# Kernel tuning notes

Measured on AMD Instinct MI355X. Metric: run time of the kernel, lower is better.

The kernel has to match this reference:

```python
import jax, jax.numpy as jnp
import numpy as np

B, N = 4, 65536
NUM_GROUP, GROUP_SIZE = 512, 64
EMB = 60


def setup_inputs() -> dict:
    key = jax.random.key(0)
    ks = jax.random.split(key, 8)
    inp = {
        'xyz': jax.random.uniform(ks[0], (B, N, 3), jnp.float32),
        'color': jax.random.uniform(ks[1], (B, N, 3), jnp.float32),
        'W1': jax.random.normal(ks[2], (6, 64), jnp.float32) * 0.2,
        'b1': jnp.zeros((64,), jnp.float32),
        'W2': jax.random.normal(ks[3], (64, 128), jnp.float32) * 0.1,
        'b2': jnp.zeros((128,), jnp.float32),
        'W3': jax.random.normal(ks[4], (128, 256), jnp.float32) * 0.08,
        'b3': jnp.zeros((256,), jnp.float32),
        'W4': jax.random.normal(ks[5], (256, 512), jnp.float32) * 0.06,
        'b4': jnp.zeros((512,), jnp.float32),
        'Wp': jax.random.normal(ks[6], (512, EMB), jnp.float32) * 0.04,
        'bp': jnp.zeros((EMB,), jnp.float32),
    }
    return inp


def fps(xyz, n):
    """Farthest point sampling. xyz: (B,N,3) -> centers (B,n,3)."""
    b, npts, _ = xyz.shape
    start = jnp.zeros((b,), jnp.int32)
    d0 = jnp.full((b, npts), 1e10, xyz.dtype)

    def step(carry, _):
        dists, last = carry
        p = jnp.take_along_axis(xyz, last[:, None, None], axis=1)  # (B,1,3)
        d = jnp.sum((xyz - p) ** 2, axis=-1)                       # (B,N)
        dists = jnp.minimum(dists, d)
        nxt = jnp.argmax(dists, axis=-1).astype(jnp.int32)
        return (dists, nxt), nxt

    (_, _), rest = jax.lax.scan(step, (d0, start), None, length=n - 1)
    idx = jnp.concatenate([start[:, None], rest.T], axis=1)        # (B,n)
    return jax.vmap(lambda pts, i: pts[i])(xyz, idx)


def knn_idx(k, xyz, new_xyz):
    """Indices of k nearest points in xyz for each query in new_xyz.
    xyz: (B,N,3), new_xyz: (B,S,3) -> (B,S,k) int32. Matches
    square_distance + topk(largest=False)."""
    sq = (jnp.sum(new_xyz ** 2, -1)[..., None]
          + jnp.sum(xyz ** 2, -1)[:, None, :]
          - 2.0 * jnp.einsum('bsc,bnc->bsn', new_xyz, xyz))        # (B,S,N)
    _, idx = jax.lax.top_k(-sq, k)
    return idx


def reference(xyz, color, W1, b1, W2, b2, W3, b3, W4, b4, Wp, bp):
    # --- Group: FPS centers + KNN neighborhood gather + centering ---
    center = fps(xyz, NUM_GROUP)                                   # (B,G,3)
    idx = knn_idx(GROUP_SIZE, xyz, center)                         # (B,G,M)
    gather = jax.vmap(lambda pts, i: pts[i])                       # pts[(B,)N,3], i (G,M)
    neighborhood = gather(xyz, idx) - center[:, :, None, :]        # (B,G,M,3) centered
    neighborhood_color = gather(color, idx)                        # (B,G,M,3)
    feats = jnp.concatenate([neighborhood, neighborhood_color], -1)  # (B,G,M,6)

    # --- PointNet: per-point MLP -> max over group -> projection ---
    x = jax.nn.relu(feats @ W1 + b1)
    x = jax.nn.relu(x @ W2 + b2)
    x = jax.nn.relu(x @ W3 + b3)
    x = jax.nn.relu(x @ W4 + b4)                                   # (B,G,M,512)
    x = jnp.max(x, axis=2)                                         # (B,G,512)
    emb = x @ Wp + bp                                              # (B,G,60)
    return emb, center
```

## Files before the change

### kernel.cpp

```cpp
#include <hip/hip_runtime.h>
#include <stdint.h>

#define DI __device__ __forceinline__

typedef _Float16 f16x8 __attribute__((ext_vector_type(8)));
typedef float f32x4 __attribute__((ext_vector_type(4)));
typedef unsigned long long u64;

constexpr int kB = 4;
constexpr int kN = 65536;
constexpr int kG = 512;
constexpr int kM = 64;
constexpr int kE = 60;
constexpr int GRD = 20;
constexpr int NCELL = GRD * GRD * GRD;
constexpr float CW = 1.0f / 20.0f;

constexpr int FPS_SUB = 8;
constexpr int FPS_TPB = 256;
constexpr int FPS_PT_T = kN / FPS_SUB / FPS_TPB;
constexpr int NFPS = kB * FPS_SUB;
constexpr int NWORK = 448;
constexpr int NBLK = NFPS + NWORK;

constexpr size_t OFF_FKEY   = 0;
constexpr size_t OFF_CCNT   = OFF_FKEY + (size_t)kB * kG * FPS_SUB * 4 * 8;
constexpr size_t OFF_GS     = OFF_CCNT + (size_t)kB * NCELL * 4;
constexpr size_t ZERO_BYTES = OFF_GS + 64;
constexpr size_t OFF_CSTART = (ZERO_BYTES + 255) & ~(size_t)255;
constexpr size_t OFF_CUR    = OFF_CSTART + (size_t)kB * (NCELL + 1) * 4;
constexpr size_t OFF_SW1    = ((OFF_CUR + (size_t)kB * NCELL * 4) + 255) & ~(size_t)255;
constexpr size_t OFF_SW2    = OFF_SW1 + 2048 * 2;
constexpr size_t OFF_SW3    = OFF_SW2 + 8192 * 2;
constexpr size_t OFF_SW4    = OFF_SW3 + 32768 * 2;
constexpr size_t OFF_WPT    = OFF_SW4 + 131072 * 2;
constexpr size_t OFF_SORT   = ((OFF_WPT + 60 * 512 * 4) + 255) & ~(size_t)255;

DI int cellof(float x) {
  int c = (int)(x * (float)GRD);
  return min(GRD - 1, max(0, c));
}
DI unsigned orderable(float f) {
  unsigned u = __float_as_uint(f);
  return (u & 0x80000000u) ? ~u : (u | 0x80000000u);
}

__global__ void k_zero(uint32_t* p, int nwords) {
  int i = blockIdx.x * blockDim.x + threadIdx.x;
  int st = gridDim.x * blockDim.x;
  for (; i < nwords; i += st) p[i] = 0u;
}

DI void swz(const float* __restrict__ W, _Float16* __restrict__ sw,
            int total, int nks, int Kreal, int N, int i0, int st) {
  for (int i = i0; i < total; i += st) {
    int j = i & 7, lane = (i >> 3) & 63, rest = i >> 9;
    int ks = rest % nks, nt = rest / nks;
    int k = ks * 32 + ((lane >> 4) << 3) + j;
    int n = nt * 16 + (lane & 15);
    sw[i] = (_Float16)((k < Kreal) ? W[k * N + n] : 0.f);
  }
}

__global__ void k_prep(const float* __restrict__ W1, const float* __restrict__ W2,
                       const float* __restrict__ W3, const float* __restrict__ W4,
                       const float* __restrict__ Wp,
                       _Float16* __restrict__ sw1, _Float16* __restrict__ sw2,
                       _Float16* __restrict__ sw3, _Float16* __restrict__ sw4,
                       float* __restrict__ wpt) {
  int i0 = blockIdx.x * blockDim.x + threadIdx.x;
  int st = gridDim.x * blockDim.x;
  swz(W1, sw1, 2048, 1, 6, 64, i0, st);
  swz(W2, sw2, 8192, 2, 64, 128, i0, st);
  swz(W3, sw3, 32768, 4, 128, 256, i0, st);
  swz(W4, sw4, 131072, 8, 256, 512, i0, st);
  for (int i = i0; i < 60 * 512; i += st) { int n = i >> 9, k = i & 511; wpt[i] = Wp[k * 60 + n]; }
}

DI void gbar(uint32_t* ctr, unsigned target) {
  __syncthreads();
  if (threadIdx.x == 0) {
    __hip_atomic_fetch_add(ctr, 1u, __ATOMIC_ACQ_REL, __HIP_MEMORY_SCOPE_AGENT);
    long bail = 0;
    while (__hip_atomic_load(ctr, __ATOMIC_ACQUIRE, __HIP_MEMORY_SCOPE_AGENT) < target) {
      __builtin_amdgcn_s_sleep(32);
      if (++bail > 100000000L) break;
    }
  }
  __syncthreads();
}

DI void fps_block(const float* __restrict__ xyz, float* __restrict__ outC,
                  u64* __restrict__ fkey, int bi) {
  const int b = bi / FPS_SUB, sub = bi % FPS_SUB;
  const int tid = threadIdx.x;
  const int wave = tid >> 6, lane = tid & 63;
  const float* X = xyz + (size_t)b * kN * 3;
  float px[FPS_PT_T], py[FPS_PT_T], pz[FPS_PT_T], dd[FPS_PT_T];
#pragma unroll
  for (int j = 0; j < FPS_PT_T; ++j) {
    int p = sub * (kN / FPS_SUB) + j * FPS_TPB + tid;
    px[j] = X[3 * p]; py[j] = X[3 * p + 1]; pz[j] = X[3 * p + 2];
    dd[j] = 1e10f;
  }
  float lx = X[0], ly = X[1], lz = X[2];
  if (sub == 0 && tid == 0) {
    outC[(size_t)b * kG * 3 + 0] = lx;
    outC[(size_t)b * kG * 3 + 1] = ly;
    outC[(size_t)b * kG * 3 + 2] = lz;
  }
  __shared__ u64 s_key[4];
  __shared__ float s_x[4], s_y[4], s_z[4];
  __shared__ float4 sp;
  u64* keyB = fkey + (size_t)b * kG * (FPS_SUB * 4);

  for (int it = 1; it < kG; ++it) {
    float bnd = -1.0f, bx = 0.f, by = 0.f, bz = 0.f;
    int bp = 0;
#pragma unroll
    for (int j = 0; j < FPS_PT_T; ++j) {
      float dx = __fsub_rn(px[j], lx);
      float dy = __fsub_rn(py[j], ly);
      float dz = __fsub_rn(pz[j], lz);
      float d = __fadd_rn(__fadd_rn(__fmul_rn(dx, dx), __fmul_rn(dy, dy)), __fmul_rn(dz, dz));
      float nd = fminf(dd[j], d);
      dd[j] = nd;
      int p = sub * (kN / FPS_SUB) + j * FPS_TPB + tid;
      if (nd > bnd) { bnd = nd; bx = px[j]; by = py[j]; bz = pz[j]; bp = p; }
    }
    u64 best = ((u64)__float_as_uint(bnd) << 32) | (unsigned)(0xFFFFFFFFu - (unsigned)bp);
#pragma unroll
    for (int off = 32; off; off >>= 1) {
      u64 ok = __shfl_down(best, (unsigned)off);
      float ox = __shfl_down(bx, (unsigned)off);
      float oy = __shfl_down(by, (unsigned)off);
      float oz = __shfl_down(bz, (unsigned)off);
      if (ok > best) { best = ok; bx = ox; by = oy; bz = oz; }
    }
    if (lane == 0) { s_key[wave] = best; s_x[wave] = bx; s_y[wave] = by; s_z[wave] = bz; }
    __syncthreads();
    if (wave == 0) {
      int i4 = lane & 3;
      u64 kk = s_key[i4]; float kx = s_x[i4], ky = s_y[i4], kz = s_z[i4];
#pragma unroll
      for (int off = 2; off; off >>= 1) {
        u64 ok = __shfl_down(kk, (unsigned)off);
        float ox = __shfl_down(kx, (unsigned)off);
        float oy = __shfl_down(ky, (unsigned)off);
        float oz = __shfl_down(kz, (unsigned)off);
        if (ok > kk) { kk = ok; kx = ox; ky = oy; kz = oz; }
      }
      u64* slots = keyB + (size_t)it * (FPS_SUB * 4);
      if (lane == 0) {
        u64 tag = (unsigned)it;
        u64* my = slots + sub * 4;
        __hip_atomic_store(my + 1, ((u64)__float_as_uint(kx) << 32) | tag,
                           __ATOMIC_RELAXED, __HIP_MEMORY_SCOPE_AGENT);
        __hip_atomic_store(my + 2, ((u64)__float_as_uint(ky) << 32) | tag,
                           __ATOMIC_RELAXED, __HIP_MEMORY_SCOPE_AGENT);
        __hip_atomic_store(my + 3, ((u64)__float_as_uint(kz) << 32) | tag,
                           __ATOMIC_RELAXED, __HIP_MEMORY_SCOPE_AGENT);
        __hip_atomic_store(my + 0, kk, __ATOMIC_RELAXED, __HIP_MEMORY_SCOPE_AGENT);
      }
      u64 v = 0; bool okp; long bail = 0;
      do {
        if (lane < FPS_SUB * 4)
          v = __hip_atomic_load(slots + lane, __ATOMIC_RELAXED, __HIP_MEMORY_SCOPE_AGENT);
        okp = (lane >= FPS_SUB * 4) ||
              ((lane & 3) ? ((unsigned)v == (unsigned)it) : (v != 0ull));
      } while (!__all(okp) && ++bail < 200000000L);
      u64 key = (lane < FPS_SUB * 4 && (lane & 3) == 0) ? v : 0ull;
      int slot = lane >> 2;
#pragma unroll
      for (int off = 16; off >= 4; off >>= 1) {
        u64 ok = __shfl_down(key, (unsigned)off);
        int os = __shfl_down(slot, (unsigned)off);
        if (ok > key) { key = ok; slot = os; }
      }
      slot = __shfl(slot, 0);
      u64 vx = __shfl(v, slot * 4 + 1);
      u64 vy = __shfl(v, slot * 4 + 2);
      u64 vz = __shfl(v, slot * 4 + 3);
      if (lane == 0) {
        float wxc = __uint_as_float((unsigned)(vx >> 32));
        float wyc = __uint_as_float((unsigned)(vy >> 32));
        float wzc = __uint_as_float((unsigned)(vz >> 32));
        sp = make_float4(wxc, wyc, wzc, 0.f);
        if (sub == 0) {
          outC[((size_t)b * kG + it) * 3 + 0] = wxc;
          outC[((size_t)b * kG + it) * 3 + 1] = wyc;
          outC[((size_t)b * kG + it) * 3 + 2] = wzc;
        }
      }
    }
    __syncthreads();
    lx = sp.x; ly = sp.y; lz = sp.z;
  }
}

DI void bitonic(u64* a, int n, int tid) {
  for (int k = 2; k <= n; k <<= 1)
    for (int j = k >> 1; j > 0; j >>= 1) {
      __syncthreads();
      for (int i = tid; i < n; i += 256) {
        int ix = i ^ j;
        if (ix > i) {
          u64 x = a[i], y = a[ix];
          bool up = ((i & k) == 0);
          if ((x > y) == up) { a[i] = y; a[ix] = x; }
        }
      }
    }
  __syncthreads();
}

template <int Kdim, int Ndim, int SIN, int SOUT>
DI void mfma_layer(const _Float16* __restrict__ Xin, _Float16* __restrict__ Xout,
                   const _Float16* __restrict__ Wsw, const float* __restrict__ bias,
                   int wave, int lane) {
  constexpr int NKS = Kdim / 32;
  constexpr int NTW = Ndim / 64;
  constexpr int CH = (NTW < 4) ? NTW : 4;
  const int quad = lane >> 4, l16 = lane & 15;
  for (int c0 = 0; c0 < NTW; c0 += CH) {
    f32x4 acc[CH][4];
#pragma unroll
    for (int nt = 0; nt < CH; ++nt) {
      float bv = bias[wave * (Ndim / 4) + (c0 + nt) * 16 + l16];
#pragma unroll
      for (int m = 0; m < 4; ++m) acc[nt][m] = {bv, bv, bv, bv};
    }
#pragma unroll
    for (int ks = 0; ks < NKS; ++ks) {
      f16x8 af[4];
#pragma unroll
      for (int m = 0; m < 4; ++m)
        af[m] = *(const f16x8*)(Xin + (m * 16 + l16) * SIN + ks * 32 + quad * 8);
#pragma unroll
      for (int nt = 0; nt < CH; ++nt) {
        int ntg = wave * NTW + c0 + nt;
        f16x8 bf = *(const f16x8*)(Wsw + ((size_t)(ntg * NKS + ks) * 64 + lane) * 8);
#pragma unroll
        for (int m = 0; m < 4; ++m)
          acc[nt][m] = __builtin_amdgcn_mfma_f32_16x16x32_f16(af[m], bf, acc[nt][m], 0, 0, 0);
      }
    }
#pragma unroll
    for (int nt = 0; nt < CH; ++nt) {
      int col = wave * (Ndim / 4) + (c0 + nt) * 16 + l16;
#pragma unroll
      for (int m = 0; m < 4; ++m)
#pragma unroll
        for (int r = 0; r < 4; ++r) {
          int row = m * 16 + quad * 4 + r;
          Xout[row * SOUT + col] = (_Float16)fmaxf(acc[nt][m][r], 0.f);
        }
    }
  }
}

DI void mfma_layer4(const _Float16* __restrict__ Xin, const _Float16* __restrict__ Wsw,
                    const float* __restrict__ bias, float* __restrict__ maxv,
                    int wave, int lane) {
  constexpr int SIN = 264, NKS = 8, NTW = 8, CH = 4;
  const int quad = lane >> 4, l16 = lane & 15;
  for (int c0 = 0; c0 < NTW; c0 += CH) {
    f32x4 acc[CH][4];
#pragma unroll
    for (int nt = 0; nt < CH; ++nt) {
      float bv = bias[wave * 128 + (c0 + nt) * 16 + l16];
#pragma unroll
      for (int m = 0; m < 4; ++m) acc[nt][m] = {bv, bv, bv, bv};
    }
#pragma unroll
    for (int ks = 0; ks < NKS; ++ks) {
      f16x8 af[4];
#pragma unroll
      for (int m = 0; m < 4; ++m)
        af[m] = *(const f16x8*)(Xin + (m * 16 + l16) * SIN + ks * 32 + quad * 8);
#pragma unroll
      for (int nt = 0; nt < CH; ++nt) {
        int ntg = wave * NTW + c0 + nt;
        f16x8 bf = *(const f16x8*)(Wsw + ((size_t)(ntg * NKS + ks) * 64 + lane) * 8);
#pragma unroll
        for (int m = 0; m < 4; ++m)
          acc[nt][m] = __builtin_amdgcn_mfma_f32_16x16x32_f16(af[m], bf, acc[nt][m], 0, 0, 0);
      }
    }
#pragma unroll
    for (int nt = 0; nt < CH; ++nt) {
      float mx = 0.f;
#pragma unroll
      for (int m = 0; m < 4; ++m)
#pragma unroll
        for (int r = 0; r < 4; ++r) mx = fmaxf(mx, acc[nt][m][r]);
      mx = fmaxf(mx, __shfl_xor(mx, 16, 64));
      mx = fmaxf(mx, __shfl_xor(mx, 32, 64));
      if (quad == 0) maxv[wave * 128 + (c0 + nt) * 16 + l16] = mx;
    }
  }
}

__global__ __launch_bounds__(256, 2) void k_fused(
    const float* __restrict__ xyz, const float* __restrict__ color,
    float* __restrict__ outC, float* __restrict__ outE,
    u64* __restrict__ fkey, uint32_t* __restrict__ ccnt,
    uint32_t* __restrict__ cstart, uint32_t* __restrict__ cur,
    float4* __restrict__ sorted, uint32_t* __restrict__ gs,
    const _Float16* __restrict__ sw1, const _Float16* __restrict__ sw2,
    const _Float16* __restrict__ sw3, const _Float16* __restrict__ sw4,
    const float* __restrict__ wpt,
    const float* __restrict__ b1, const float* __restrict__ b2,
    const float* __restrict__ b3, const float* __restrict__ b4,
    const float* __restrict__ bp) {
  const int bi = blockIdx.x;
  if (bi < NFPS) { fps_block(xyz, outC, fkey, bi); return; }

  const int wj = bi - NFPS;
  const int tid = threadIdx.x;
  const int wave = tid >> 6, lane = tid & 63;
  __shared__ __align__(16) char smem[65536];
  __shared__ int nC;
  __shared__ float4 spc;
  __shared__ uint32_t s_part[256];
  u64* cand = (u64*)smem;

  for (int i = wj * 256 + tid; i < kB * kN; i += NWORK * 256) {
    int b = i >> 16, p = i & (kN - 1);
    const float* q = xyz + ((size_t)b * kN + p) * 3;
    int cid = (cellof(q[2]) * GRD + cellof(q[1])) * GRD + cellof(q[0]);
    atomicAdd(&ccnt[b * NCELL + cid], 1u);
  }
  gbar(gs + 0, NWORK);
  if (wj < kB) {
    int b = wj;
    const uint32_t* cc = ccnt + (size_t)b * NCELL;
    uint32_t* cs = cstart + (size_t)b * (NCELL + 1);
    uint32_t* cu = cur + (size_t)b * NCELL;
    const int chunk = 32;
    int c0 = tid * chunk;
    uint32_t s = 0;
    for (int i = 0; i < chunk; ++i) { int c = c0 + i; if (c < NCELL) s += cc[c]; }
    s_part[tid] = s;
    __syncthreads();
    for (int off = 1; off < 256; off <<= 1) {
      uint32_t add = (tid >= off) ? s_part[tid - off] : 0u;
      __syncthreads();
      s_part[tid] += add;
      __syncthreads();
    }
    uint32_t run = s_part[tid] - s;
    for (int i = 0; i < chunk; ++i) {
      int c = c0 + i;
      if (c < NCELL) { cs[c] = run; cu[c] = run; run += cc[c]; }
    }
    if (tid == 255) cs[NCELL] = run;
  }
  gbar(gs + 1, NWORK);
  for (int i = wj * 256 + tid; i < kB * kN; i += NWORK * 256) {
    int b = i >> 16, p = i & (kN - 1);
    const float* q = xyz + ((size_t)b * kN + p) * 3;
    float x = q[0], y = q[1], z = q[2];
    int cid = (cellof(z) * GRD + cellof(y)) * GRD + cellof(x);
    uint32_t pos = atomicAdd(&cur[b * NCELL + cid], 1u);
    sorted[(size_t)b * kN + pos] = make_float4(x, y, z, __uint_as_float((unsigned)p));
  }
  gbar(gs + 2, NWORK);

  for (int j = wj; j < kB * kG; j += NWORK) {
    const int it = j >> 2, b = j & 3;
    const float* X = xyz + (size_t)b * kN * 3;
    if (it == 0) {
      if (tid == 0) spc = make_float4(X[0], X[1], X[2], 0.f);
    } else if (tid < 64) {
      const u64* slots = fkey + ((size_t)b * kG + it) * (FPS_SUB * 4);
      const int pl = tid;
      u64 v = 0; bool okp; long bail = 0;
      for (;;) {
        if (pl < FPS_SUB * 4)
          v = __hip_atomic_load(slots + pl, __ATOMIC_RELAXED, __HIP_MEMORY_SCOPE_AGENT);
        okp = (pl >= FPS_SUB * 4) ||
              ((pl & 3) ? ((unsigned)v == (unsigned)it) : (v != 0ull));
        if (__all(okp)) break;
        __builtin_amdgcn_s_sleep(127);
        if (++bail > 50000000L) break;
      }
      u64 key = (pl < FPS_SUB * 4 && (pl & 3) == 0) ? v : 0ull;
      int slot = pl >> 2;
#pragma unroll
      for (int off = 16; off >= 4; off >>= 1) {
        u64 ok = __shfl_down(key, (unsigned)off);
        int os = __shfl_down(slot, (unsigned)off);
        if (ok > key) { key = ok; slot = os; }
      }
      slot = __shfl(slot, 0);
      u64 vx = __shfl(v, slot * 4 + 1);
      u64 vy = __shfl(v, slot * 4 + 2);
      u64 vz = __shfl(v, slot * 4 + 3);
      if (pl == 0)
        spc = make_float4(__uint_as_float((unsigned)(vx >> 32)),
                          __uint_as_float((unsigned)(vy >> 32)),
                          __uint_as_float((unsigned)(vz >> 32)), 0.f);
    }
    __syncthreads();
    const float cx = spc.x, cy = spc.y, cz = spc.z;

    const float nc = __fadd_rn(__fadd_rn(__fmul_rn(cx, cx), __fmul_rn(cy, cy)), __fmul_rn(cz, cz));
    const float4* SP = sorted + (size_t)b * kN;
    const uint32_t* CS = cstart + (size_t)b * (NCELL + 1);
    const int ccx = cellof(cx), ccy = cellof(cy), ccz = cellof(cz);
    if (tid == 0) nC = 0;
    __syncthreads();
    int plox = 1, phix = 0, ploy = 1, phiy = 0, ploz = 1, phiz = 0;
    for (int r = 1; r <= GRD; ++r) {
      int lox = max(0, ccx - r), hix = min(GRD - 1, ccx + r);
      int loy = max(0, ccy - r), hiy = min(GRD - 1, ccy + r);
      int loz = max(0, ccz - r), hiz = min(GRD - 1, ccz + r);
      for (int z = loz; z <= hiz; ++z)
        for (int y = loy; y <= hiy; ++y) {
          bool rowPrev = (r > 1) && (z >= ploz && z <= phiz && y >= ploy && y <= phiy);
          for (int s = 0; s < 2; ++s) {
            int xa, xb;
            if (!rowPrev) { if (s) break; xa = lox; xb = hix; }
            else if (s == 0) { xa = lox; xb = plox - 1; }
            else { xa = phix + 1; xb = hix; }
            if (xa > xb) continue;
            int c0 = (z * GRD + y) * GRD + xa;
            int i0 = CS[c0];
            int i1 = CS[(z * GRD + y) * GRD + xb + 1];
            for (int i = i0 + tid; i < i1; i += 256) {
              float4 pt = SP[i];
              float npn = __fadd_rn(__fadd_rn(__fmul_rn(pt.x, pt.x), __fmul_rn(pt.y, pt.y)),
                                    __fmul_rn(pt.z, pt.z));
              float dot = __fadd_rn(__fadd_rn(__fmul_rn(cx, pt.x), __fmul_rn(cy, pt.y)),
                                    __fmul_rn(cz, pt.z));
              float sq = __fsub_rn(__fadd_rn(nc, npn), __fmul_rn(2.0f, dot));
              unsigned key = orderable(sq);
              int pos = atomicAdd(&nC, 1);
              if (pos < 8192)
                cand[pos] = ((u64)key << 32) | (unsigned)__float_as_uint(pt.w);
            }
          }
        }
      __syncthreads();
      int n = min(nC, 8192);
      float rc = 1e30f;
      if (lox > 0) rc = fminf(rc, cx - (float)lox * CW);
      if (hix < GRD - 1) rc = fminf(rc, (float)(hix + 1) * CW - cx);
      if (loy > 0) rc = fminf(rc, cy - (float)loy * CW);
      if (hiy < GRD - 1) rc = fminf(rc, (float)(hiy + 1) * CW - cy);
      if (loz > 0) rc = fminf(rc, cz - (float)loz * CW);
      if (hiz < GRD - 1) rc = fminf(rc, (float)(hiz + 1) * CW - cz);
      float r2 = (rc >= 1e29f) ? 3.0e38f : rc * rc * (1.0f - 1e-5f);
      unsigned keyR = orderable(r2);
      bool done = false;
      if (n >= kM) {
        int np2 = 1;
        while (np2 < n) np2 <<= 1;
        for (int i = n + tid; i < np2; i += 256) cand[i] = ~0ull;
        bitonic(cand, np2, tid);
        unsigned k63 = (unsigned)(cand[kM - 1] >> 32);
        done = (k63 <= keyR);
        if (tid == 0) nC = n;
      }
      __syncthreads();
      if (done) break;
      plox = lox; phix = hix; ploy = loy; phiy = hiy; ploz = loz; phiz = hiz;
    }

    uint32_t pidx = 0;
    if (tid < kM) pidx = (uint32_t)(cand[tid] & 0xFFFFFFFFu);
    __syncthreads();
    _Float16* bufA = (_Float16*)smem;
    _Float16* bufB = (_Float16*)(smem + 17408);
    float* maxv = (float*)smem;
    float* psum = (float*)(smem + 2048);
    if (tid < kM) {
      const float* xp = xyz + ((size_t)b * kN + pidx) * 3;
      const float* cp = color + ((size_t)b * kN + pidx) * 3;
      f16x8 v = {};
      v[0] = (_Float16)__fsub_rn(xp[0], cx);
      v[1] = (_Float16)__fsub_rn(xp[1], cy);
      v[2] = (_Float16)__fsub_rn(xp[2], cz);
      v[3] = (_Float16)cp[0];
      v[4] = (_Float16)cp[1];
      v[5] = (_Float16)cp[2];
      f16x8 zf = {};
      *(f16x8*)(bufA + tid * 40 + 0) = v;
      *(f16x8*)(bufA + tid * 40 + 8) = zf;
      *(f16x8*)(bufA + tid * 40 + 16) = zf;
      *(f16x8*)(bufA + tid * 40 + 24) = zf;
    }
    __syncthreads();
    mfma_layer<32, 64, 40, 72>(bufA, bufB, sw1, b1, wave, lane);
    __syncthreads();
    mfma_layer<64, 128, 72, 136>(bufB, bufA, sw2, b2, wave, lane);
    __syncthreads();
    mfma_layer<128, 256, 136, 264>(bufA, bufB, sw3, b3, wave, lane);
    __syncthreads();
    mfma_layer4(bufB, sw4, b4, maxv, wave, lane);
    __syncthreads();
    if (tid < 240) {
      int jj = tid >> 2, q = tid & 3;
      const float* w = wpt + (size_t)jj * 512 + q * 128;
      float s = 0.f;
#pragma unroll 4
      for (int k = 0; k < 128; ++k) s = fmaf(maxv[q * 128 + k], w[k], s);
      psum[tid] = s;
    }
    __syncthreads();
    if (tid < kE) {
      float e = __fadd_rn(__fadd_rn(psum[tid * 4 + 0], psum[tid * 4 + 1]),
                          __fadd_rn(psum[tid * 4 + 2], psum[tid * 4 + 3])) + bp[tid];
      outE[((size_t)b * kG + it) * kE + tid] = e;
    }
    __syncthreads();
  }
}

extern "C" void kernel_launch(void* const* d_in, const int* in_sizes, int n_in,
                              void* d_out, int out_size, void* d_ws, size_t ws_size,
                              hipStream_t stream) {
  (void)in_sizes; (void)n_in; (void)out_size; (void)ws_size;
  const float* xyz = (const float*)d_in[0];
  const float* color = (const float*)d_in[1];
  const float* W1 = (const float*)d_in[2];
  const float* b1 = (const float*)d_in[3];
  const float* W2 = (const float*)d_in[4];
  const float* b2 = (const float*)d_in[5];
  const float* W3 = (const float*)d_in[6];
  const float* b3 = (const float*)d_in[7];
  const float* W4 = (const float*)d_in[8];
  const float* b4 = (const float*)d_in[9];
  const float* Wp = (const float*)d_in[10];
  const float* bp = (const float*)d_in[11];

  char* ws = (char*)d_ws;
  auto fkey = (u64*)(ws + OFF_FKEY);
  auto ccnt = (uint32_t*)(ws + OFF_CCNT);
  auto gs = (uint32_t*)(ws + OFF_GS);
  auto cstart = (uint32_t*)(ws + OFF_CSTART);
  auto cur = (uint32_t*)(ws + OFF_CUR);
  auto sw1 = (_Float16*)(ws + OFF_SW1);
  auto sw2 = (_Float16*)(ws + OFF_SW2);
  auto sw3 = (_Float16*)(ws + OFF_SW3);
  auto sw4 = (_Float16*)(ws + OFF_SW4);
  auto wpt = (float*)(ws + OFF_WPT);
  auto sorted = (float4*)(ws + OFF_SORT);

  float* outE = (float*)d_out;
  float* outC = outE + (size_t)kB * kG * kE;

  k_zero<<<128, 256, 0, stream>>>((uint32_t*)ws, (int)(ZERO_BYTES / 4));
  k_prep<<<256, 256, 0, stream>>>(W1, W2, W3, W4, Wp, sw1, sw2, sw3, sw4, wpt);
  k_fused<<<NBLK, 256, 0, stream>>>(xyz, color, outC, outE, fkey, ccnt, cstart, cur,
                                    sorted, gs, sw1, sw2, sw3, sw4, wpt,
                                    b1, b2, b3, b4, bp);
}
```

Baseline: 2.128 ms.

## Replace brute-force multi-block FPS with single-block chunk-pruned FPS over grid-sorted points

```diff
diff --git a/kernel.cpp b/kernel.cpp
--- a/kernel.cpp
+++ b/kernel.cpp
@@ -6,6 +6,7 @@
 typedef _Float16 f16x8 __attribute__((ext_vector_type(8)));
 typedef float f32x4 __attribute__((ext_vector_type(4)));
 typedef unsigned long long u64;
+typedef unsigned short u16;
 
 constexpr int kB = 4;
 constexpr int kN = 65536;
@@ -16,20 +17,18 @@
 constexpr int NCELL = GRD * GRD * GRD;
 constexpr float CW = 1.0f / 20.0f;
 
-constexpr int FPS_SUB = 8;
-constexpr int FPS_TPB = 256;
-constexpr int FPS_PT_T = kN / FPS_SUB / FPS_TPB;
-constexpr int NFPS = kB * FPS_SUB;
-constexpr int NWORK = 448;
+constexpr int NCH = 2048;
+constexpr int CHSZ = 32;
+constexpr int NFPS = kB;
+constexpr int NWORK = 508;
 constexpr int NBLK = NFPS + NWORK;
 
-constexpr size_t OFF_FKEY   = 0;
-constexpr size_t OFF_CCNT   = OFF_FKEY + (size_t)kB * kG * FPS_SUB * 4 * 8;
-constexpr size_t OFF_GS     = OFF_CCNT + (size_t)kB * NCELL * 4;
-constexpr size_t ZERO_BYTES = OFF_GS + 64;
+constexpr size_t OFF_CLINE  = 0;
+constexpr size_t OFF_GRDY   = (size_t)kB * kG * 128;
+constexpr size_t ZERO_BYTES = OFF_GRDY + 64;
 constexpr size_t OFF_CSTART = (ZERO_BYTES + 255) & ~(size_t)255;
-constexpr size_t OFF_CUR    = OFF_CSTART + (size_t)kB * (NCELL + 1) * 4;
-constexpr size_t OFF_SW1    = ((OFF_CUR + (size_t)kB * NCELL * 4) + 255) & ~(size_t)255;
+constexpr size_t OFF_DD     = (OFF_CSTART + (size_t)kB * (NCELL + 1) * 4 + 255) & ~(size_t)255;
+constexpr size_t OFF_SW1    = (OFF_DD + (size_t)kB * kN * 4 + 255) & ~(size_t)255;
 constexpr size_t OFF_SW2    = OFF_SW1 + 2048 * 2;
 constexpr size_t OFF_SW3    = OFF_SW2 + 8192 * 2;
 constexpr size_t OFF_SW4    = OFF_SW3 + 32768 * 2;
@@ -43,6 +42,16 @@
 DI unsigned orderable(float f) {
   unsigned u = __float_as_uint(f);
   return (u & 0x80000000u) ? ~u : (u | 0x80000000u);
+}
+DI _Float16 f16dn(float v) {
+  _Float16 h = (_Float16)v;
+  if ((float)h > v) h = __builtin_bit_cast(_Float16, (u16)(__builtin_bit_cast(u16, h) - 1));
+  return h;
+}
+DI _Float16 f16up(float v) {
+  _Float16 h = (_Float16)v;
+  if ((float)h < v) h = __builtin_bit_cast(_Float16, (u16)(__builtin_bit_cast(u16, h) + 1));
+  return h;
 }
 
 __global__ void k_zero(uint32_t* p, int nwords) {
@@ -77,127 +86,6 @@
   for (int i = i0; i < 60 * 512; i += st) { int n = i >> 9, k = i & 511; wpt[i] = Wp[k * 60 + n]; }
 }
 
-DI void gbar(uint32_t* ctr, unsigned target) {
-  __syncthreads();
-  if (threadIdx.x == 0) {
-    __hip_atomic_fetch_add(ctr, 1u, __ATOMIC_ACQ_REL, __HIP_MEMORY_SCOPE_AGENT);
-    long bail = 0;
-    while (__hip_atomic_load(ctr, __ATOMIC_ACQUIRE, __HIP_MEMORY_SCOPE_AGENT) < target) {
-      __builtin_amdgcn_s_sleep(32);
-      if (++bail > 100000000L) break;
-    }
-  }
-  __syncthreads();
-}
-
-DI void fps_block(const float* __restrict__ xyz, float* __restrict__ outC,
-                  u64* __restrict__ fkey, int bi) {
-  const int b = bi / FPS_SUB, sub = bi % FPS_SUB;
-  const int tid = threadIdx.x;
-  const int wave = tid >> 6, lane = tid & 63;
-  const float* X = xyz + (size_t)b * kN * 3;
-  float px[FPS_PT_T], py[FPS_PT_T], pz[FPS_PT_T], dd[FPS_PT_T];
-#pragma unroll
-  for (int j = 0; j < FPS_PT_T; ++j) {
-    int p = sub * (kN / FPS_SUB) + j * FPS_TPB + tid;
-    px[j] = X[3 * p]; py[j] = X[3 * p + 1]; pz[j] = X[3 * p + 2];
-    dd[j] = 1e10f;
-  }
-  float lx = X[0], ly = X[1], lz = X[2];
-  if (sub == 0 && tid == 0) {
-    outC[(size_t)b * kG * 3 + 0] = lx;
-    outC[(size_t)b * kG * 3 + 1] = ly;
-    outC[(size_t)b * kG * 3 + 2] = lz;
-  }
-  __shared__ u64 s_key[4];
-  __shared__ float s_x[4], s_y[4], s_z[4];
-  __shared__ float4 sp;
-  u64* keyB = fkey + (size_t)b * kG * (FPS_SUB * 4);
-
-  for (int it = 1; it < kG; ++it) {
-    float bnd = -1.0f, bx = 0.f, by = 0.f, bz = 0.f;
-    int bp = 0;
-#pragma unroll
-    for (int j = 0; j < FPS_PT_T; ++j) {
-      float dx = __fsub_rn(px[j], lx);
-      float dy = __fsub_rn(py[j], ly);
-      float dz = __fsub_rn(pz[j], lz);
-      float d = __fadd_rn(__fadd_rn(__fmul_rn(dx, dx), __fmul_rn(dy, dy)), __fmul_rn(dz, dz));
-      float nd = fminf(dd[j], d);
-      dd[j] = nd;
-      int p = sub * (kN / FPS_SUB) + j * FPS_TPB + tid;
-      if (nd > bnd) { bnd = nd; bx = px[j]; by = py[j]; bz = pz[j]; bp = p; }
-    }
-    u64 best = ((u64)__float_as_uint(bnd) << 32) | (unsigned)(0xFFFFFFFFu - (unsigned)bp);
-#pragma unroll
-    for (int off = 32; off; off >>= 1) {
-      u64 ok = __shfl_down(best, (unsigned)off);
-      float ox = __shfl_down(bx, (unsigned)off);
-      float oy = __shfl_down(by, (unsigned)off);
-      float oz = __shfl_down(bz, (unsigned)off);
-      if (ok > best) { best = ok; bx = ox; by = oy; bz = oz; }
-    }
-    if (lane == 0) { s_key[wave] = best; s_x[wave] = bx; s_y[wave] = by; s_z[wave] = bz; }
-    __syncthreads();
-    if (wave == 0) {
-      int i4 = lane & 3;
-      u64 kk = s_key[i4]; float kx = s_x[i4], ky = s_y[i4], kz = s_z[i4];
-#pragma unroll
-      for (int off = 2; off; off >>= 1) {
-        u64 ok = __shfl_down(kk, (unsigned)off);
-        float ox = __shfl_down(kx, (unsigned)off);
-        float oy = __shfl_down(ky, (unsigned)off);
-        float oz = __shfl_down(kz, (unsigned)off);
-        if (ok > kk) { kk = ok; kx = ox; ky = oy; kz = oz; }
-      }
-      u64* slots = keyB + (size_t)it * (FPS_SUB * 4);
-      if (lane == 0) {
-        u64 tag = (unsigned)it;
-        u64* my = slots + sub * 4;
-        __hip_atomic_store(my + 1, ((u64)__float_as_uint(kx) << 32) | tag,
-                           __ATOMIC_RELAXED, __HIP_MEMORY_SCOPE_AGENT);
-        __hip_atomic_store(my + 2, ((u64)__float_as_uint(ky) << 32) | tag,
-                           __ATOMIC_RELAXED, __HIP_MEMORY_SCOPE_AGENT);
-        __hip_atomic_store(my + 3, ((u64)__float_as_uint(kz) << 32) | tag,
-                           __ATOMIC_RELAXED, __HIP_MEMORY_SCOPE_AGENT);
-        __hip_atomic_store(my + 0, kk, __ATOMIC_RELAXED, __HIP_MEMORY_SCOPE_AGENT);
-      }
-      u64 v = 0; bool okp; long bail = 0;
-      do {
-        if (lane < FPS_SUB * 4)
-          v = __hip_atomic_load(slots + lane, __ATOMIC_RELAXED, __HIP_MEMORY_SCOPE_AGENT);
-        okp = (lane >= FPS_SUB * 4) ||
-              ((lane & 3) ? ((unsigned)v == (unsigned)it) : (v != 0ull));
-      } while (!__all(okp) && ++bail < 200000000L);
-      u64 key = (lane < FPS_SUB * 4 && (lane & 3) == 0) ? v : 0ull;
-      int slot = lane >> 2;
-#pragma unroll
-      for (int off = 16; off >= 4; off >>= 1) {
-        u64 ok = __shfl_down(key, (unsigned)off);
-        int os = __shfl_down(slot, (unsigned)off);
-        if (ok > key) { key = ok; slot = os; }
-      }
-      slot = __shfl(slot, 0);
-      u64 vx = __shfl(v, slot * 4 + 1);
-      u64 vy = __shfl(v, slot * 4 + 2);
-      u64 vz = __shfl(v, slot * 4 + 3);
-      if (lane == 0) {
-        float wxc = __uint_as_float((unsigned)(vx >> 32));
-        float wyc = __uint_as_float((unsigned)(vy >> 32));
-        float wzc = __uint_as_float((unsigned)(vz >> 32));
-        sp = make_float4(wxc, wyc, wzc, 0.f);
-        if (sub == 0) {
-          outC[((size_t)b * kG + it) * 3 + 0] = wxc;
-          outC[((size_t)b * kG + it) * 3 + 1] = wyc;
-          outC[((size_t)b * kG + it) * 3 + 2] = wzc;
-        }
-      }
-    }
-    __syncthreads();
-    lx = sp.x; ly = sp.y; lz = sp.z;
-  }
-}
-
 DI void bitonic(u64* a, int n, int tid) {
   for (int k = 2; k <= n; k <<= 1)
     for (int j = k >> 1; j > 0; j >>= 1) {
@@ -301,112 +189,261 @@
   }
 }
 
+DI void fps_block(const float* __restrict__ xyz, float* __restrict__ outC,
+                  u64* __restrict__ cline, uint32_t* __restrict__ grdy,
+                  uint32_t* __restrict__ cstart_g, float4* __restrict__ sorted_g,
+                  float* __restrict__ dd_g, int b, char* smem) {
+  __builtin_amdgcn_s_setprio(3);
+  const int tid = threadIdx.x;
+  const int wave = tid >> 6, lane = tid & 63;
+  const int h = tid >> 5, sub = tid & 31;
+  const float* X = xyz + (size_t)b * kN * 3;
+  float4* SP = sorted_g + (size_t)b * kN;
+  float* DD = dd_g + (size_t)b * kN;
+  u64* cl = cline + (size_t)b * kG * 16;
+
+  u64* ckey = (u64*)smem;
+  float* cxyz = (float*)(smem + 16384);
+  _Float16* cbb = (_Float16*)(smem + 40960);
+  u16* queue = (u16*)(smem + 65536);
+  int* qn = (int*)(smem + 69632);
+  u64* warr_key = (u64*)(smem + 69640);
+  int* warr_cid = (int*)(smem + 69672);
+  float4* wslot = (float4*)(smem + 69696);
+
+  {
+    uint32_t* ccnt = (uint32_t*)smem;
+    uint32_t* cur = (uint32_t*)(smem + 32768);
+    uint32_t* spart = (uint32_t*)(smem + 65536);
+    for (int i = tid; i < 8192; i += 256) ccnt[i] = 0u;
+    __syncthreads();
+    for (int i = tid; i < kN; i += 256) {
+      float x = X[3 * i], y = X[3 * i + 1], z = X[3 * i + 2];
+      int cid = (cellof(z) * GRD + cellof(y)) * GRD + cellof(x);
+      atomicAdd(&ccnt[cid], 1u);
+    }
+    __syncthreads();
+    uint32_t* cs = cstart_g + (size_t)b * (NCELL + 1);
+    const int chunk = 32;
+    int c0 = tid * chunk;
+    uint32_t s = 0;
+    for (int i = 0; i < chunk; ++i) s += ccnt[c0 + i];
+    spart[tid] = s;
+    __syncthreads();
+    for (int off = 1; off < 256; off <<= 1) {
+      uint32_t add = (tid >= off) ? spart[tid - off] : 0u;
+      __syncthreads();
+      spart[tid] += add;
+      __syncthreads();
+    }
+    uint32_t run = spart[tid] - s;
+    for (int i = 0; i < chunk; ++i) {
+      int c = c0 + i;
+      uint32_t cc = ccnt[c];
+      cur[c] = run;
+      if (c < NCELL) cs[c] = run;
+      run += cc;
+    }
+    if (tid == 255) cs[NCELL] = run;
+    __syncthreads();
+    for (int i = tid; i < kN; i += 256) {
+      float x = X[3 * i], y = X[3 * i + 1], z = X[3 * i + 2];
+      int cid = (cellof(z) * GRD + cellof(y)) * GRD + cellof(x);
+      uint32_t pos = atomicAdd(&cur[cid], 1u);
+      SP[pos] = make_float4(x, y, z, __uint_as_float((unsigned)i));
+    }
+    __syncthreads();
+    for (int c = h; c < NCH; c += 8) {
+      float4 p = SP[c * CHSZ + sub];
+      float mnx = p.x, mxx = p.x, mny = p.y, mxy = p.y, mnz = p.z, mxz = p.z;
+#pragma unroll
+      for (int off = 16; off; off >>= 1) {
+        mnx = fminf(mnx, __shfl_down(mnx, (unsigned)off));
+        mxx = fmaxf(mxx, __shfl_down(mxx, (unsigned)off));
+        mny = fminf(mny, __shfl_down(mny, (unsigned)off));
+        mxy = fmaxf(mxy, __shfl_down(mxy, (unsigned)off));
+        mnz = fminf(mnz, __shfl_down(mnz, (unsigned)off));
+        mxz = fmaxf(mxz, __shfl_down(mxz, (unsigned)off));
+      }
+      if (sub == 0) {
+        cbb[c * 6 + 0] = f16dn(mnx); cbb[c * 6 + 1] = f16up(mxx);
+        cbb[c * 6 + 2] = f16dn(mny); cbb[c * 6 + 3] = f16up(mxy);
+        cbb[c * 6 + 4] = f16dn(mnz); cbb[c * 6 + 5] = f16up(mxz);
+      }
+    }
+    __syncthreads();
+  }
+  __threadfence();
+  __syncthreads();
+  float cx = X[0], cy = X[1], cz = X[2];
+  if (tid == 0) {
+    __hip_atomic_store(grdy + b, 1u, __ATOMIC_RELEASE, __HIP_MEMORY_SCOPE_AGENT);
+    u64 tg = 1u;
+    __hip_atomic_store(cl + 0, ((u64)__float_as_uint(cx) << 32) | tg, __ATOMIC_RELAXED, __HIP_MEMORY_SCOPE_AGENT);
+    __hip_atomic_store(cl + 1, ((u64)__float_as_uint(cy) << 32) | tg, __ATOMIC_RELAXED, __HIP_MEMORY_SCOPE_AGENT);
+    __hip_atomic_store(cl + 2, ((u64)__float_as_uint(cz) << 32) | tg, __ATOMIC_RELAXED, __HIP_MEMORY_SCOPE_AGENT);
+    outC[(size_t)b * kG * 3 + 0] = cx;
+    outC[(size_t)b * kG * 3 + 1] = cy;
+    outC[(size_t)b * kG * 3 + 2] = cz;
+    *qn = 0;
+  }
+  __syncthreads();
+
+  for (int it = 1; it < kG; ++it) {
+    if (it > 1) {
+#pragma unroll
+      for (int i = 0; i < 8; ++i) {
+        int c = tid + 256 * i;
+        int c6 = c * 6;
+        float lox = (float)cbb[c6 + 0], hix = (float)cbb[c6 + 1];
+        float loy = (float)cbb[c6 + 2], hiy = (float)cbb[c6 + 3];
+        float loz = (float)cbb[c6 + 4], hiz = (float)cbb[c6 + 5];
+        float dx = fmaxf(fmaxf(lox - cx, cx - hix), 0.f);
+        float dy = fmaxf(fmaxf(loy - cy, cy - hiy), 0.f);
+        float dz = fmaxf(fmaxf(loz - cz, cz - hiz), 0.f);
+        float lb = dx * dx + dy * dy + dz * dz;
+        float ub = __uint_as_float((unsigned)(ckey[c] >> 32));
+        if (!(lb * 0.999f > ub)) {
+          int pos = atomicAdd(qn, 1);
+          queue[pos] = (u16)c;
+        }
+      }
+    }
+    __syncthreads();
+    {
+      const int Q = (it == 1) ? NCH : *qn;
+      const bool first = (it == 1);
+      for (int t = h; t < Q; t += 8) {
+        int c = first ? t : (int)queue[t];
+        int gidx = c * CHSZ + sub;
+        float4 p = SP[gidx];
+        float ddo = first ? 1e10f : DD[gidx];
+        float dx = __fsub_rn(p.x, cx);
+        float dy = __fsub_rn(p.y, cy);
+        float dz = __fsub_rn(p.z, cz);
+        float d = __fadd_rn(__fadd_rn(__fmul_rn(dx, dx), __fmul_rn(dy, dy)), __fmul_rn(dz, dz));
+        float nd = fminf(ddo, d);
+        DD[gidx] = nd;
+        u64 key = ((u64)__float_as_uint(nd) << 32) |
+                  (u64)(0xFFFFFFFFu - (unsigned)__float_as_uint(p.w));
+        float bx = p.x, by = p.y, bz = p.z;
+#pragma unroll
+        for (int off = 16; off; off >>= 1) {
+          u64 ok = __shfl_down(key, (unsigned)off);
+          float ox = __shfl_down(bx, (unsigned)off);
+          float oy = __shfl_down(by, (unsigned)off);
+          float oz = __shfl_down(bz, (unsigned)off);
+          if (ok > key) { key = ok; bx = ox; by = oy; bz = oz; }
+        }
+        if (sub == 0) {
+          ckey[c] = key;
+          cxyz[c * 3 + 0] = bx; cxyz[c * 3 + 1] = by; cxyz[c * 3 + 2] = bz;
+        }
+      }
+    }
+    __syncthreads();
+    {
+      u64 key = 0ull; int cid = 0;
+#pragma unroll
+      for (int i = 0; i < 8; ++i) {
+        int c = tid + 256 * i;
+        u64 k = ckey[c];
+        if (k > key) { key = k; cid = c; }
+      }
+#pragma unroll
+      for (int off = 32; off; off >>= 1) {
+        u64 ok = __shfl_down(key, (unsigned)off);
+        int oc = __shfl_down(cid, (unsigned)off);
+        if (ok > key) { key = ok; cid = oc; }
+      }
+      if (lane == 0) { warr_key[wave] = key; warr_cid[wave] = cid; }
+    }
+    __syncthreads();
+    if (tid == 0) {
+      u64 key = warr_key[0]; int cid = warr_cid[0];
+#pragma unroll
+      for (int i = 1; i < 4; ++i)
+        if (warr_key[i] > key) { key = warr_key[i]; cid = warr_cid[i]; }
+      float wx = cxyz[cid * 3 + 0], wy = cxyz[cid * 3 + 1], wz = cxyz[cid * 3 + 2];
+      *wslot = make_float4(wx, wy, wz, 0.f);
+      u64 tg = (unsigned)(it + 1);
+      __hip_atomic_store(cl + (size_t)it * 16 + 0, ((u64)__float_as_uint(wx) << 32) | tg, __ATOMIC_RELAXED, __HIP_MEMORY_SCOPE_AGENT);
+      __hip_atomic_store(cl + (size_t)it * 16 + 1, ((u64)__float_as_uint(wy) << 32) | tg, __ATOMIC_RELAXED, __HIP_MEMORY_SCOPE_AGENT);
+      __hip_atomic_store(cl + (size_t)it * 16 + 2, ((u64)__float_as_uint(wz) << 32) | tg, __ATOMIC_RELAXED, __HIP_MEMORY_SCOPE_AGENT);
+      outC[((size_t)b * kG + it) * 3 + 0] = wx;
+      outC[((size_t)b * kG + it) * 3 + 1] = wy;
+      outC[((size_t)b * kG + it) * 3 + 2] = wz;
+      *qn = 0;
+    }
+    __syncthreads();
+    float4 wc = *wslot;
+    cx = wc.x; cy = wc.y; cz = wc.z;
+  }
+}
+
 __global__ __launch_bounds__(256, 2) void k_fused(
     const float* __restrict__ xyz, const float* __restrict__ color,
     float* __restrict__ outC, float* __restrict__ outE,
-    u64* __restrict__ fkey, uint32_t* __restrict__ ccnt,
-    uint32_t* __restrict__ cstart, uint32_t* __restrict__ cur,
-    float4* __restrict__ sorted, uint32_t* __restrict__ gs,
+    u64* __restrict__ cline, uint32_t* __restrict__ grdy,
+    uint32_t* __restrict__ cstart, float4* __restrict__ sorted,
+    float* __restrict__ dd_g,
     const _Float16* __restrict__ sw1, const _Float16* __restrict__ sw2,
     const _Float16* __restrict__ sw3, const _Float16* __restrict__ sw4,
     const float* __restrict__ wpt,
     const float* __restrict__ b1, const float* __restrict__ b2,
     const float* __restrict__ b3, const float* __restrict__ b4,
     const float* __restrict__ bp) {
+  __shared__ __align__(16) char smem[69760];
   const int bi = blockIdx.x;
-  if (bi < NFPS) { fps_block(xyz, outC, fkey, bi); return; }
+  if (bi < NFPS) {
+    fps_block(xyz, outC, cline, grdy, cstart, sorted, dd_g, bi, smem);
+    return;
+  }
 
   const int wj = bi - NFPS;
   const int tid = threadIdx.x;
   const int wave = tid >> 6, lane = tid & 63;
-  __shared__ __align__(16) char smem[65536];
   __shared__ int nC;
   __shared__ float4 spc;
-  __shared__ uint32_t s_part[256];
   u64* cand = (u64*)smem;
 
-  for (int i = wj * 256 + tid; i < kB * kN; i += NWORK * 256) {
-    int b = i >> 16, p = i & (kN - 1);
-    const float* q = xyz + ((size_t)b * kN + p) * 3;
-    int cid = (cellof(q[2]) * GRD + cellof(q[1])) * GRD + cellof(q[0]);
-    atomicAdd(&ccnt[b * NCELL + cid], 1u);
-  }
-  gbar(gs + 0, NWORK);
-  if (wj < kB) {
-    int b = wj;
-    const uint32_t* cc = ccnt + (size_t)b * NCELL;
-    uint32_t* cs = cstart + (size_t)b * (NCELL + 1);
-    uint32_t* cu = cur + (size_t)b * NCELL;
-    const int chunk = 32;
-    int c0 = tid * chunk;
-    uint32_t s = 0;
-    for (int i = 0; i < chunk; ++i) { int c = c0 + i; if (c < NCELL) s += cc[c]; }
-    s_part[tid] = s;
-    __syncthreads();
-    for (int off = 1; off < 256; off <<= 1) {
-      uint32_t add = (tid >= off) ? s_part[tid - off] : 0u;
-      __syncthreads();
-      s_part[tid] += add;
-      __syncthreads();
-    }
-    uint32_t run = s_part[tid] - s;
-    for (int i = 0; i < chunk; ++i) {
-      int c = c0 + i;
-      if (c < NCELL) { cs[c] = run; cu[c] = run; run += cc[c]; }
-    }
-    if (tid == 255) cs[NCELL] = run;
-  }
-  gbar(gs + 1, NWORK);
-  for (int i = wj * 256 + tid; i < kB * kN; i += NWORK * 256) {
-    int b = i >> 16, p = i & (kN - 1);
-    const float* q = xyz + ((size_t)b * kN + p) * 3;
-    float x = q[0], y = q[1], z = q[2];
-    int cid = (cellof(z) * GRD + cellof(y)) * GRD + cellof(x);
-    uint32_t pos = atomicAdd(&cur[b * NCELL + cid], 1u);
-    sorted[(size_t)b * kN + pos] = make_float4(x, y, z, __uint_as_float((unsigned)p));
-  }
-  gbar(gs + 2, NWORK);
+  if (tid < 64) {
+    long bail = 0;
+    for (;;) {
+      uint32_t g = 1u;
+      if (lane < kB)
+        g = __hip_atomic_load(grdy + lane, __ATOMIC_ACQUIRE, __HIP_MEMORY_SCOPE_AGENT);
+      if (__all(g == 1u)) break;
+      __builtin_amdgcn_s_sleep(64);
+      if (++bail > 50000000L) break;
+    }
+  }
+  __syncthreads();
 
   for (int j = wj; j < kB * kG; j += NWORK) {
     const int it = j >> 2, b = j & 3;
-    const float* X = xyz + (size_t)b * kN * 3;
-    if (it == 0) {
-      if (tid == 0) spc = make_float4(X[0], X[1], X[2], 0.f);
-    } else if (tid < 64) {
-      const u64* slots = fkey + ((size_t)b * kG + it) * (FPS_SUB * 4);
-      const int pl = tid;
-      u64 v = 0; bool okp; long bail = 0;
+    if (tid < 64) {
+      const u64* e = cline + ((size_t)b * kG + it) * 16;
+      u64 v = 0; long bail = 0;
       for (;;) {
-        if (pl < FPS_SUB * 4)
-          v = __hip_atomic_load(slots + pl, __ATOMIC_RELAXED, __HIP_MEMORY_SCOPE_AGENT);
-        okp = (pl >= FPS_SUB * 4) ||
-              ((pl & 3) ? ((unsigned)v == (unsigned)it) : (v != 0ull));
-        if (__all(okp)) break;
-        __builtin_amdgcn_s_sleep(127);
-        if (++bail > 50000000L) break;
-      }
-      u64 key = (pl < FPS_SUB * 4 && (pl & 3) == 0) ? v : 0ull;
-      int slot = pl >> 2;
-#pragma unroll
-      for (int off = 16; off >= 4; off >>= 1) {
-        u64 ok = __shfl_down(key, (unsigned)off);
-        int os = __shfl_down(slot, (unsigned)off);
-        if (ok > key) { key = ok; slot = os; }
-      }
-      slot = __shfl(slot, 0);
-      u64 vx = __shfl(v, slot * 4 + 1);
-      u64 vy = __shfl(v, slot * 4 + 2);
-      u64 vz = __shfl(v, slot * 4 + 3);
-      if (pl == 0)
-        spc = make_float4(__uint_as_float((unsigned)(vx >> 32)),
-                          __uint_as_float((unsigned)(vy >> 32)),
-                          __uint_as_float((unsigned)(vz >> 32)), 0.f);
+        if (lane < 3)
+          v = __hip_atomic_load(e + lane, __ATOMIC_RELAXED, __HIP_MEMORY_SCOPE_AGENT);
+        bool ok = (lane >= 3) || ((unsigned)v == (unsigned)(it + 1));
+        if (__all(ok)) break;
+        __builtin_amdgcn_s_sleep(8);
+        if (++bail > 100000000L) break;
+      }
+      u64 v0 = __shfl(v, 0), v1 = __shfl(v, 1), v2 = __shfl(v, 2);
+      if (tid == 0)
+        spc = make_float4(__uint_as_float((unsigned)(v0 >> 32)),
+                          __uint_as_float((unsigned)(v1 >> 32)),
+                          __uint_as_float((unsigned)(v2 >> 32)), 0.f);
     }
     __syncthreads();
     const float cx = spc.x, cy = spc.y, cz = spc.z;
 
     const float nc = __fadd_rn(__fadd_rn(__fmul_rn(cx, cx), __fmul_rn(cy, cy)), __fmul_rn(cz, cz));
-    const float4* SP = sorted + (size_t)b * kN;
+    const float4* SPb = sorted + (size_t)b * kN;
     const uint32_t* CS = cstart + (size_t)b * (NCELL + 1);
     const int ccx = cellof(cx), ccy = cellof(cy), ccz = cellof(cz);
     if (tid == 0) nC = 0;
@@ -429,7 +466,7 @@
             int i0 = CS[c0];
             int i1 = CS[(z * GRD + y) * GRD + xb + 1];
             for (int i = i0 + tid; i < i1; i += 256) {
-              float4 pt = SP[i];
+              float4 pt = SPb[i];
               float npn = __fadd_rn(__fadd_rn(__fmul_rn(pt.x, pt.x), __fmul_rn(pt.y, pt.y)),
                                     __fmul_rn(pt.z, pt.z));
               float dot = __fadd_rn(__fadd_rn(__fmul_rn(cx, pt.x), __fmul_rn(cy, pt.y)),
@@ -536,11 +573,10 @@
   const float* bp = (const float*)d_in[11];
 
   char* ws = (char*)d_ws;
-  auto fkey = (u64*)(ws + OFF_FKEY);
-  auto ccnt = (uint32_t*)(ws + OFF_CCNT);
-  auto gs = (uint32_t*)(ws + OFF_GS);
+  auto cline = (u64*)(ws + OFF_CLINE);
+  auto grdy = (uint32_t*)(ws + OFF_GRDY);
   auto cstart = (uint32_t*)(ws + OFF_CSTART);
-  auto cur = (uint32_t*)(ws + OFF_CUR);
+  auto dd = (float*)(ws + OFF_DD);
   auto sw1 = (_Float16*)(ws + OFF_SW1);
   auto sw2 = (_Float16*)(ws + OFF_SW2);
   auto sw3 = (_Float16*)(ws + OFF_SW3);
@@ -553,7 +589,7 @@
 
   k_zero<<<128, 256, 0, stream>>>((uint32_t*)ws, (int)(ZERO_BYTES / 4));
   k_prep<<<256, 256, 0, stream>>>(W1, W2, W3, W4, Wp, sw1, sw2, sw3, sw4, wpt);
-  k_fused<<<NBLK, 256, 0, stream>>>(xyz, color, outC, outE, fkey, ccnt, cstart, cur,
-                                    sorted, gs, sw1, sw2, sw3, sw4, wpt,
+  k_fused<<<NBLK, 256, 0, stream>>>(xyz, color, outC, outE, cline, grdy, cstart,
+                                    sorted, dd, sw1, sw2, sw3, sw4, wpt,
                                     b1, b2, b3, b4, bp);
 }
```

Result: slower. 7.262 ms (+241.2%).

## Double FPS sub-blocks, publish centers via single cache line, interleave FPS blocks

Applied to the files above, without the earlier changes.

```diff
diff --git a/kernel.cpp b/kernel.cpp
--- a/kernel.cpp
+++ b/kernel.cpp
@@ -16,15 +16,15 @@
 constexpr int NCELL = GRD * GRD * GRD;
 constexpr float CW = 1.0f / 20.0f;
 
-constexpr int FPS_SUB = 8;
+constexpr int FPS_SUB = 16;
 constexpr int FPS_TPB = 256;
 constexpr int FPS_PT_T = kN / FPS_SUB / FPS_TPB;
-constexpr int NFPS = kB * FPS_SUB;
 constexpr int NWORK = 448;
-constexpr int NBLK = NFPS + NWORK;
+constexpr int NBLK = 512;
 
 constexpr size_t OFF_FKEY   = 0;
-constexpr size_t OFF_CCNT   = OFF_FKEY + (size_t)kB * kG * FPS_SUB * 4 * 8;
+constexpr size_t OFF_CLINE  = OFF_FKEY + (size_t)kB * kG * FPS_SUB * 4 * 8;
+constexpr size_t OFF_CCNT   = OFF_CLINE + (size_t)kB * kG * 128;
 constexpr size_t OFF_GS     = OFF_CCNT + (size_t)kB * NCELL * 4;
 constexpr size_t ZERO_BYTES = OFF_GS + 64;
 constexpr size_t OFF_CSTART = (ZERO_BYTES + 255) & ~(size_t)255;
@@ -91,8 +91,8 @@
 }
 
 DI void fps_block(const float* __restrict__ xyz, float* __restrict__ outC,
-                  u64* __restrict__ fkey, int bi) {
-  const int b = bi / FPS_SUB, sub = bi % FPS_SUB;
+                  u64* __restrict__ fkey, u64* __restrict__ cline, int b, int sub) {
+  __builtin_amdgcn_s_setprio(3);
   const int tid = threadIdx.x;
   const int wave = tid >> 6, lane = tid & 63;
   const float* X = xyz + (size_t)b * kN * 3;
@@ -104,10 +104,15 @@
     dd[j] = 1e10f;
   }
   float lx = X[0], ly = X[1], lz = X[2];
+  u64* cl = cline + (size_t)b * kG * 16;
   if (sub == 0 && tid == 0) {
     outC[(size_t)b * kG * 3 + 0] = lx;
     outC[(size_t)b * kG * 3 + 1] = ly;
     outC[(size_t)b * kG * 3 + 2] = lz;
+    u64 tg = 1u;
+    __hip_atomic_store(cl + 0, ((u64)__float_as_uint(lx) << 32) | tg, __ATOMIC_RELAXED, __HIP_MEMORY_SCOPE_AGENT);
+    __hip_atomic_store(cl + 1, ((u64)__float_as_uint(ly) << 32) | tg, __ATOMIC_RELAXED, __HIP_MEMORY_SCOPE_AGENT);
+    __hip_atomic_store(cl + 2, ((u64)__float_as_uint(lz) << 32) | tg, __ATOMIC_RELAXED, __HIP_MEMORY_SCOPE_AGENT);
   }
   __shared__ u64 s_key[4];
   __shared__ float s_x[4], s_y[4], s_z[4];
@@ -164,15 +169,13 @@
       }
       u64 v = 0; bool okp; long bail = 0;
       do {
-        if (lane < FPS_SUB * 4)
-          v = __hip_atomic_load(slots + lane, __ATOMIC_RELAXED, __HIP_MEMORY_SCOPE_AGENT);
-        okp = (lane >= FPS_SUB * 4) ||
-              ((lane & 3) ? ((unsigned)v == (unsigned)it) : (v != 0ull));
-      } while (!__all(okp) && ++bail < 200000000L);
-      u64 key = (lane < FPS_SUB * 4 && (lane & 3) == 0) ? v : 0ull;
+        v = __hip_atomic_load(slots + lane, __ATOMIC_RELAXED, __HIP_MEMORY_SCOPE_AGENT);
+        okp = (lane & 3) ? ((unsigned)v == (unsigned)it) : (v != 0ull);
+      } while (!__all(okp) && ++bail < 100000000L);
+      u64 key = ((lane & 3) == 0) ? v : 0ull;
       int slot = lane >> 2;
 #pragma unroll
-      for (int off = 16; off >= 4; off >>= 1) {
+      for (int off = 32; off; off >>= 1) {
         u64 ok = __shfl_down(key, (unsigned)off);
         int os = __shfl_down(slot, (unsigned)off);
         if (ok > key) { key = ok; slot = os; }
@@ -190,6 +193,11 @@
           outC[((size_t)b * kG + it) * 3 + 0] = wxc;
           outC[((size_t)b * kG + it) * 3 + 1] = wyc;
           outC[((size_t)b * kG + it) * 3 + 2] = wzc;
+          u64 tg = (unsigned)(it + 1);
+          u64* e = cl + (size_t)it * 16;
+          __hip_atomic_store(e + 0, ((u64)__float_as_uint(wxc) << 32) | tg, __ATOMIC_RELAXED, __HIP_MEMORY_SCOPE_AGENT);
+          __hip_atomic_store(e + 1, ((u64)__float_as_uint(wyc) << 32) | tg, __ATOMIC_RELAXED, __HIP_MEMORY_SCOPE_AGENT);
+          __hip_atomic_store(e + 2, ((u64)__float_as_uint(wzc) << 32) | tg, __ATOMIC_RELAXED, __HIP_MEMORY_SCOPE_AGENT);
         }
       }
     }
@@ -304,9 +312,10 @@
 __global__ __launch_bounds__(256, 2) void k_fused(
     const float* __restrict__ xyz, const float* __restrict__ color,
     float* __restrict__ outC, float* __restrict__ outE,
-    u64* __restrict__ fkey, uint32_t* __restrict__ ccnt,
-    uint32_t* __restrict__ cstart, uint32_t* __restrict__ cur,
-    float4* __restrict__ sorted, uint32_t* __restrict__ gs,
+    u64* __restrict__ fkey, u64* __restrict__ cline,
+    uint32_t* __restrict__ ccnt, uint32_t* __restrict__ cstart,
+    uint32_t* __restrict__ cur, float4* __restrict__ sorted,
+    uint32_t* __restrict__ gs,
     const _Float16* __restrict__ sw1, const _Float16* __restrict__ sw2,
     const _Float16* __restrict__ sw3, const _Float16* __restrict__ sw4,
     const float* __restrict__ wpt,
@@ -314,9 +323,12 @@
     const float* __restrict__ b3, const float* __restrict__ b4,
     const float* __restrict__ bp) {
   const int bi = blockIdx.x;
-  if (bi < NFPS) { fps_block(xyz, outC, fkey, bi); return; }
-
-  const int wj = bi - NFPS;
+  if (bi < 128 && (bi & 7) < kB) {
+    fps_block(xyz, outC, fkey, cline, bi & 7, bi >> 3);
+    return;
+  }
+
+  const int wj = (bi < 128) ? ((bi >> 3) * 4 + ((bi & 7) - kB)) : (64 + (bi - 128));
   const int tid = threadIdx.x;
   const int wave = tid >> 6, lane = tid & 63;
   __shared__ __align__(16) char smem[65536];
@@ -369,44 +381,28 @@
 
   for (int j = wj; j < kB * kG; j += NWORK) {
     const int it = j >> 2, b = j & 3;
-    const float* X = xyz + (size_t)b * kN * 3;
-    if (it == 0) {
-      if (tid == 0) spc = make_float4(X[0], X[1], X[2], 0.f);
-    } else if (tid < 64) {
-      const u64* slots = fkey + ((size_t)b * kG + it) * (FPS_SUB * 4);
-      const int pl = tid;
-      u64 v = 0; bool okp; long bail = 0;
+    if (tid < 64) {
+      const u64* e = cline + ((size_t)b * kG + it) * 16;
+      u64 v = 0; long bail = 0;
       for (;;) {
-        if (pl < FPS_SUB * 4)
-          v = __hip_atomic_load(slots + pl, __ATOMIC_RELAXED, __HIP_MEMORY_SCOPE_AGENT);
-        okp = (pl >= FPS_SUB * 4) ||
-              ((pl & 3) ? ((unsigned)v == (unsigned)it) : (v != 0ull));
-        if (__all(okp)) break;
-        __builtin_amdgcn_s_sleep(127);
-        if (++bail > 50000000L) break;
-      }
-      u64 key = (pl < FPS_SUB * 4 && (pl & 3) == 0) ? v : 0ull;
-      int slot = pl >> 2;
-#pragma unroll
-      for (int off = 16; off >= 4; off >>= 1) {
-        u64 ok = __shfl_down(key, (unsigned)off);
-        int os = __shfl_down(slot, (unsigned)off);
-        if (ok > key) { key = ok; slot = os; }
-      }
-      slot = __shfl(slot, 0);
-      u64 vx = __shfl(v, slot * 4 + 1);
-      u64 vy = __shfl(v, slot * 4 + 2);
-      u64 vz = __shfl(v, slot * 4 + 3);
-      if (pl == 0)
-        spc = make_float4(__uint_as_float((unsigned)(vx >> 32)),
-                          __uint_as_float((unsigned)(vy >> 32)),
-                          __uint_as_float((unsigned)(vz >> 32)), 0.f);
+        if (lane < 3)
+          v = __hip_atomic_load(e + lane, __ATOMIC_RELAXED, __HIP_MEMORY_SCOPE_AGENT);
+        bool ok = (lane >= 3) || ((unsigned)v == (unsigned)(it + 1));
+        if (__all(ok)) break;
+        __builtin_amdgcn_s_sleep(8);
+        if (++bail > 100000000L) break;
+      }
+      u64 v0 = __shfl(v, 0), v1 = __shfl(v, 1), v2 = __shfl(v, 2);
+      if (tid == 0)
+        spc = make_float4(__uint_as_float((unsigned)(v0 >> 32)),
+                          __uint_as_float((unsigned)(v1 >> 32)),
+                          __uint_as_float((unsigned)(v2 >> 32)), 0.f);
     }
     __syncthreads();
     const float cx = spc.x, cy = spc.y, cz = spc.z;
 
     const float nc = __fadd_rn(__fadd_rn(__fmul_rn(cx, cx), __fmul_rn(cy, cy)), __fmul_rn(cz, cz));
-    const float4* SP = sorted + (size_t)b * kN;
+    const float4* SPb = sorted + (size_t)b * kN;
     const uint32_t* CS = cstart + (size_t)b * (NCELL + 1);
     const int ccx = cellof(cx), ccy = cellof(cy), ccz = cellof(cz);
     if (tid == 0) nC = 0;
@@ -429,7 +425,7 @@
             int i0 = CS[c0];
             int i1 = CS[(z * GRD + y) * GRD + xb + 1];
             for (int i = i0 + tid; i < i1; i += 256) {
-              float4 pt = SP[i];
+              float4 pt = SPb[i];
               float npn = __fadd_rn(__fadd_rn(__fmul_rn(pt.x, pt.x), __fmul_rn(pt.y, pt.y)),
                                     __fmul_rn(pt.z, pt.z));
               float dot = __fadd_rn(__fadd_rn(__fmul_rn(cx, pt.x), __fmul_rn(cy, pt.y)),
@@ -537,6 +533,7 @@
 
   char* ws = (char*)d_ws;
   auto fkey = (u64*)(ws + OFF_FKEY);
+  auto cline = (u64*)(ws + OFF_CLINE);
   auto ccnt = (uint32_t*)(ws + OFF_CCNT);
   auto gs = (uint32_t*)(ws + OFF_GS);
   auto cstart = (uint32_t*)(ws + OFF_CSTART);
@@ -551,9 +548,9 @@
   float* outE = (float*)d_out;
   float* outC = outE + (size_t)kB * kG * kE;
 
-  k_zero<<<128, 256, 0, stream>>>((uint32_t*)ws, (int)(ZERO_BYTES / 4));
+  k_zero<<<256, 256, 0, stream>>>((uint32_t*)ws, (int)(ZERO_BYTES / 4));
   k_prep<<<256, 256, 0, stream>>>(W1, W2, W3, W4, Wp, sw1, sw2, sw3, sw4, wpt);
-  k_fused<<<NBLK, 256, 0, stream>>>(xyz, color, outC, outE, fkey, ccnt, cstart, cur,
-                                    sorted, gs, sw1, sw2, sw3, sw4, wpt,
+  k_fused<<<NBLK, 256, 0, stream>>>(xyz, color, outC, outE, fkey, cline, ccnt, cstart,
+                                    cur, sorted, gs, sw1, sw2, sw3, sw4, wpt,
                                     b1, b2, b3, b4, bp);
 }
```

New measurement: 2.122 ms. Within noise of the previous version (-0.3%).
